# Kernel tuning notes

Hardware: AMD Instinct MI355X
Metric: run time of the kernel (lower is better)

## Reference

```python
import jax, jax.numpy as jnp
import numpy as np

DIM = 768
H = 12
HD = DIM // H
SCALE = HD ** (-0.5)


def setup_inputs() -> dict:
    key = jax.random.key(0)
    ks = jax.random.split(key, 10)
    s = DIM ** (-0.5)
    x = jax.random.normal(ks[0], (8, 1024, DIM), dtype=jnp.float32)
    Wq = jax.random.normal(ks[1], (DIM, DIM), dtype=jnp.float32) * s
    Wk = jax.random.normal(ks[2], (DIM, DIM), dtype=jnp.float32) * s
    Wv = jax.random.normal(ks[3], (DIM, DIM), dtype=jnp.float32) * s
    Wl = jax.random.normal(ks[4], (H, H), dtype=jnp.float32) * (H ** -0.5)
    bl = jax.random.normal(ks[5], (H,), dtype=jnp.float32) * 0.02
    Ww = jax.random.normal(ks[6], (H, H), dtype=jnp.float32) * (H ** -0.5)
    bw = jax.random.normal(ks[7], (H,), dtype=jnp.float32) * 0.02
    Wp = jax.random.normal(ks[8], (DIM, DIM), dtype=jnp.float32) * s
    bp = jax.random.normal(ks[9], (DIM,), dtype=jnp.float32) * 0.02
    return {"x": x, "Wq": Wq, "Wk": Wk, "Wv": Wv, "Wl": Wl, "bl": bl,
            "Ww": Ww, "bw": bw, "Wp": Wp, "bp": bp}


def reference(x, Wq, Wk, Wv, Wl, bl, Ww, bw, Wp, bp):
    B, N, C = x.shape
    # QKV projections (no bias), split heads -> (B, H, N, hd)
    q = (x @ Wq).reshape(B, N, H, HD).transpose(0, 2, 1, 3) * SCALE
    k = (x @ Wk).reshape(B, N, H, HD).transpose(0, 2, 1, 3)
    v = (x @ Wv).reshape(B, N, H, HD).transpose(0, 2, 1, 3)
    # scores: (B, H, N, N)
    attn = jnp.einsum('bhid,bhjd->bhij', q, k)
    # talking heads pre-softmax: mix over head axis (Linear on last dim of BNNH)
    attn = jnp.einsum('bhij,gh->bgij', attn, Wl) + bl[None, :, None, None]
    attn = jax.nn.softmax(attn, axis=-1)
    # talking heads post-softmax
    attn = jnp.einsum('bhij,gh->bgij', attn, Ww) + bw[None, :, None, None]
    out = jnp.einsum('bhij,bhjd->bhid', attn, v)  # (B, H, N, hd)
    out = out.transpose(0, 2, 1, 3).reshape(B, N, C)
    return out @ Wp + bp
```

## Files before the change

### kernel.cpp

```cpp
#include <hip/hip_runtime.h>
#include <hip/hip_bf16.h>

#define DIM 768
#define NH 12
#define HD 64
#define SEQ 1024
#define BATCH 8

typedef __bf16 bf16x8 __attribute__((ext_vector_type(8)));
typedef _Float16 f16x4 __attribute__((ext_vector_type(4)));
typedef float f32x4 __attribute__((ext_vector_type(4)));

__global__ __launch_bounds__(256) void xcvt(
    const float* __restrict__ X, __bf16* __restrict__ Xb)
{
  const size_t i = ((size_t)blockIdx.x * 256 + threadIdx.x) * 8;
  float4 a0 = *(const float4*)(X + i);
  float4 a1 = *(const float4*)(X + i + 4);
  bf16x8 v = { (__bf16)a0.x, (__bf16)a0.y, (__bf16)a0.z, (__bf16)a0.w,
               (__bf16)a1.x, (__bf16)a1.y, (__bf16)a1.z, (__bf16)a1.w };
  *(bf16x8*)(Xb + i) = v;
}

__global__ __launch_bounds__(256) void wtrans(
    const float* __restrict__ Wq, const float* __restrict__ Wk,
    const float* __restrict__ Wv, const float* __restrict__ Wp,
    __bf16* __restrict__ Tq, __bf16* __restrict__ Tk,
    __bf16* __restrict__ Tv, __bf16* __restrict__ Tp)
{
  const int z = blockIdx.z;
  const float* W = (z==0) ? Wq : (z==1) ? Wk : (z==2) ? Wv : Wp;
  __bf16* T = (z==0) ? Tq : (z==1) ? Tk : (z==2) ? Tv : Tp;
  __shared__ float tile[32][33];
  const int t = threadIdx.x, tx = t & 31, ty = t >> 5;
  const int k0 = blockIdx.y * 32, n0 = blockIdx.x * 32;
#pragma unroll
  for (int u = 0; u < 4; ++u)
    tile[ty + u*8][tx] = W[(size_t)(k0 + ty + u*8) * DIM + n0 + tx];
  __syncthreads();
#pragma unroll
  for (int u = 0; u < 4; ++u)
    T[(size_t)(n0 + ty + u*8) * DIM + k0 + tx] = (__bf16)tile[tx][ty + u*8];
}

__global__ __launch_bounds__(256) void gemm_qkv(
    const __bf16* __restrict__ Xb, const __bf16* __restrict__ WT,
    __bf16* __restrict__ Qo, __bf16* __restrict__ Ko, _Float16* __restrict__ Vt2)
{
  __shared__ __bf16 As[128 * 40];
  __shared__ __bf16 Bs[128 * 40];

  const int t = threadIdx.x, lane = t & 63, w = t >> 6;
  const int n16 = lane & 15, q = lane >> 4;
  const int m0 = blockIdx.y * 128, n0 = blockIdx.x * 128;
  const int wm = (w >> 1) * 64, wn = (w & 1) * 64;

  const int srow = t >> 2, scol = (t & 3) * 8;
  const __bf16* Ag = Xb + (size_t)(m0 + srow) * DIM + scol;
  const __bf16* Bg = WT + (size_t)(n0 + srow) * DIM + scol;

  f32x4 acc[4][4];
#pragma unroll
  for (int mt = 0; mt < 4; ++mt)
#pragma unroll
    for (int nt = 0; nt < 4; ++nt) acc[mt][nt] = (f32x4){0.f,0.f,0.f,0.f};

  for (int kb = 0; kb < DIM; kb += 32) {
    __syncthreads();
    bf16x8 a0 = *(const bf16x8*)(Ag + kb);
    bf16x8 a1 = *(const bf16x8*)(Ag + (size_t)64 * DIM + kb);
    bf16x8 b0 = *(const bf16x8*)(Bg + kb);
    bf16x8 b1 = *(const bf16x8*)(Bg + (size_t)64 * DIM + kb);
    *(bf16x8*)&As[srow * 40 + scol] = a0;
    *(bf16x8*)&As[(srow + 64) * 40 + scol] = a1;
    *(bf16x8*)&Bs[srow * 40 + scol] = b0;
    *(bf16x8*)&Bs[(srow + 64) * 40 + scol] = b1;
    __syncthreads();

    bf16x8 af[4], bg[4];
#pragma unroll
    for (int mt = 0; mt < 4; ++mt)
      af[mt] = *(const bf16x8*)&As[(wm + mt*16 + n16) * 40 + q*8];
#pragma unroll
    for (int nt = 0; nt < 4; ++nt)
      bg[nt] = *(const bf16x8*)&Bs[(wn + nt*16 + n16) * 40 + q*8];
#pragma unroll
    for (int mt = 0; mt < 4; ++mt)
#pragma unroll
      for (int nt = 0; nt < 4; ++nt)
        acc[mt][nt] = __builtin_amdgcn_mfma_f32_16x16x32_bf16(af[mt], bg[nt], acc[mt][nt], 0, 0, 0);
  }

#pragma unroll
  for (int nt = 0; nt < 4; ++nt) {
    const int n = n0 + wn + nt*16 + n16;
    const int z = n / DIM, c = n % DIM;
    const int h = c >> 6, d = c & 63;
#pragma unroll
    for (int mt = 0; mt < 4; ++mt) {
#pragma unroll
      for (int r = 0; r < 4; ++r) {
        const int row = m0 + wm + mt*16 + q*4 + r;
        const int bb = row >> 10, ii = row & 1023;
        const float v = acc[mt][nt][r];
        if (z == 0)
          Qo[(((size_t)bb*NH + h)*SEQ + ii)*HD + d] = (__bf16)(v * 0.125f);
        else if (z == 1)
          Ko[(((size_t)bb*NH + h)*SEQ + ii)*HD + d] = (__bf16)v;
        else
          Vt2[((((size_t)bb*NH + h)*64 + (ii >> 4))*HD + d)*16 + (ii & 15)] = (_Float16)v;
      }
    }
  }
}

__global__ __launch_bounds__(256, 2) void attn_fused(
    const __bf16* __restrict__ Qg, const __bf16* __restrict__ Kg,
    const _Float16* __restrict__ Vt2,
    const float* __restrict__ Wl, const float* __restrict__ bl,
    const float* __restrict__ Ww, const float* __restrict__ bw,
    __bf16* __restrict__ Aout)
{
  __shared__ float Sl[2][12][324];
  __shared__ _Float16 Pl[2][16 * 248];

  const int t = threadIdx.x, lane = t & 63, w = t >> 6;
  const int n16 = lane & 15, q = lane >> 4;
  const int h0 = w * 3;
  const int b = blockIdx.y, i0 = blockIdx.x * 16;
  const size_t bbase = (size_t)b * NH * SEQ * HD;

  f16x4 wlA, wwA;
  f32x4 blC, bwC;
#pragma unroll
  for (int j = 0; j < 4; ++j) {
    const int k = q*4 + j;
    wlA[j] = (n16 < 12 && k < 12) ? (_Float16)Wl[n16*12 + k] : (_Float16)0.f;
    wwA[j] = (n16 < 12 && k < 12) ? (_Float16)Ww[n16*12 + k] : (_Float16)0.f;
    blC[j] = (k < 12) ? bl[k] : 0.f;
    bwC[j] = (k < 12) ? bw[k] : 0.f;
  }

  bf16x8 qf[3][2];
#pragma unroll
  for (int hh = 0; hh < 3; ++hh)
#pragma unroll
    for (int cc = 0; cc < 2; ++cc)
      qf[hh][cc] = *(const bf16x8*)(Qg + bbase + ((size_t)(h0+hh)*SEQ + i0 + n16)*HD + cc*32 + q*8);

  const f32x4 z4 = {0.f, 0.f, 0.f, 0.f};

  float lrun[4][4];
#pragma unroll
  for (int c = 0; c < 4; ++c)
#pragma unroll
    for (int r = 0; r < 4; ++r) lrun[c][r] = 0.f;

  bf16x8 kC[3][2], kN[3][2];
#pragma unroll
  for (int hh = 0; hh < 3; ++hh) {
    const __bf16* kp = Kg + bbase + ((size_t)(h0+hh)*SEQ + n16)*HD + q*8;
    kC[hh][0] = *(const bf16x8*)kp;
    kC[hh][1] = *(const bf16x8*)(kp + 32);
  }

#pragma unroll 2
  for (int jt = 0; jt < SEQ/16; ++jt) {
    const int buf = jt & 1;
    const int jn = (jt < SEQ/16 - 1) ? jt + 1 : jt;
#pragma unroll
    for (int hh = 0; hh < 3; ++hh) {
      const __bf16* kp = Kg + bbase + ((size_t)(h0+hh)*SEQ + jn*16 + n16)*HD + q*8;
      kN[hh][0] = *(const bf16x8*)kp;
      kN[hh][1] = *(const bf16x8*)(kp + 32);
    }
#pragma unroll
    for (int hh = 0; hh < 3; ++hh) {
      f32x4 s = __builtin_amdgcn_mfma_f32_16x16x32_bf16(kC[hh][0], qf[hh][0], z4, 0, 0, 0);
      s = __builtin_amdgcn_mfma_f32_16x16x32_bf16(kC[hh][1], qf[hh][1], s, 0, 0, 0);
      *(f32x4*)&Sl[buf][h0+hh][n16*20 + q*4] = s;
    }
    __syncthreads();
#pragma unroll
    for (int c = 0; c < 4; ++c) {
      const int i = w*4 + c;
      f16x4 sf;
#pragma unroll
      for (int dd = 0; dd < 4; ++dd) {
        int h = q*4 + dd; if (h > 11) h = 11;
        sf[dd] = (_Float16)Sl[buf][h][i*20 + n16];
      }
      f32x4 sm = __builtin_amdgcn_mfma_f32_16x16x16f16(wlA, sf, blC, 0, 0, 0);
#pragma unroll
      for (int r = 0; r < 4; ++r) lrun[c][r] += __expf(sm[r]);
    }
#pragma unroll
    for (int hh = 0; hh < 3; ++hh) { kC[hh][0] = kN[hh][0]; kC[hh][1] = kN[hh][1]; }
  }

  float linv[4][4];
#pragma unroll
  for (int c = 0; c < 4; ++c)
#pragma unroll
    for (int r = 0; r < 4; ++r) {
      float l = lrun[c][r];
      l += __shfl_xor(l, 1);
      l += __shfl_xor(l, 2);
      l += __shfl_xor(l, 4);
      l += __shfl_xor(l, 8);
      linv[c][r] = 1.0f / l;
    }

  f32x4 oacc[3][4];
#pragma unroll
  for (int hh = 0; hh < 3; ++hh)
#pragma unroll
    for (int dc = 0; dc < 4; ++dc) oacc[hh][dc] = z4;

  f16x4 vC[3][4], vN[3][4];
#pragma unroll
  for (int hh = 0; hh < 3; ++hh) {
    const __bf16* kp = Kg + bbase + ((size_t)(h0+hh)*SEQ + n16)*HD + q*8;
    kC[hh][0] = *(const bf16x8*)kp;
    kC[hh][1] = *(const bf16x8*)(kp + 32);
  }

#pragma unroll 2
  for (int jt = 0; jt < SEQ/16; ++jt) {
    const int buf = jt & 1;
    const int jn = (jt < SEQ/16 - 1) ? jt + 1 : jt;
#pragma unroll
    for (int hh = 0; hh < 3; ++hh) {
      const __bf16* kp = Kg + bbase + ((size_t)(h0+hh)*SEQ + jn*16 + n16)*HD + q*8;
      kN[hh][0] = *(const bf16x8*)kp;
      kN[hh][1] = *(const bf16x8*)(kp + 32);
    }
#pragma unroll
    for (int hh = 0; hh < 3; ++hh) {
      const _Float16* vb = Vt2 + (((size_t)(b*NH + h0 + hh)*64 + jt)*HD)*16;
#pragma unroll
      for (int dc = 0; dc < 4; ++dc)
        vN[hh][dc] = *(const f16x4*)(vb + (size_t)(dc*16 + n16)*16 + q*4);
    }
#pragma unroll
    for (int hh = 0; hh < 3; ++hh) {
      f32x4 s = __builtin_amdgcn_mfma_f32_16x16x32_bf16(kC[hh][0], qf[hh][0], z4, 0, 0, 0);
      s = __builtin_amdgcn_mfma_f32_16x16x32_bf16(kC[hh][1], qf[hh][1], s, 0, 0, 0);
      *(f32x4*)&Sl[buf][h0+hh][n16*20 + q*4] = s;
    }
    __syncthreads();
#pragma unroll
    for (int c = 0; c < 4; ++c) {
      const int i = w*4 + c;
      f16x4 sf;
#pragma unroll
      for (int dd = 0; dd < 4; ++dd) {
        int h = q*4 + dd; if (h > 11) h = 11;
        sf[dd] = (_Float16)Sl[buf][h][i*20 + n16];
      }
      f32x4 sm = __builtin_amdgcn_mfma_f32_16x16x16f16(wlA, sf, blC, 0, 0, 0);
      f16x4 pnf;
#pragma unroll
      for (int r = 0; r < 4; ++r)
        pnf[r] = (_Float16)(__expf(sm[r]) * linv[c][r]);
      f32x4 p2 = __builtin_amdgcn_mfma_f32_16x16x16f16(wwA, pnf, bwC, 0, 0, 0);
      if (q < 3) {
#pragma unroll
        for (int r = 0; r < 4; ++r)
          Pl[buf][i*248 + (q*4 + r)*20 + n16] = (_Float16)p2[r];
      }
    }
    if (jt > 0) {
#pragma unroll
      for (int hh = 0; hh < 3; ++hh) {
        const int g2 = h0 + hh;
        f16x4 pa = *(const f16x4*)&Pl[1 - buf][n16*248 + g2*20 + q*4];
#pragma unroll
        for (int dc = 0; dc < 4; ++dc)
          oacc[hh][dc] = __builtin_amdgcn_mfma_f32_16x16x16f16(pa, vC[hh][dc], oacc[hh][dc], 0, 0, 0);
      }
    }
#pragma unroll
    for (int hh = 0; hh < 3; ++hh) {
      kC[hh][0] = kN[hh][0]; kC[hh][1] = kN[hh][1];
#pragma unroll
      for (int dc = 0; dc < 4; ++dc) vC[hh][dc] = vN[hh][dc];
    }
  }
  __syncthreads();
#pragma unroll
  for (int hh = 0; hh < 3; ++hh) {
    const int g2 = h0 + hh;
    f16x4 pa = *(const f16x4*)&Pl[1][n16*248 + g2*20 + q*4];
#pragma unroll
    for (int dc = 0; dc < 4; ++dc)
      oacc[hh][dc] = __builtin_amdgcn_mfma_f32_16x16x16f16(pa, vC[hh][dc], oacc[hh][dc], 0, 0, 0);
  }

#pragma unroll
  for (int hh = 0; hh < 3; ++hh)
#pragma unroll
    for (int dc = 0; dc < 4; ++dc)
#pragma unroll
      for (int r = 0; r < 4; ++r)
        Aout[((size_t)(b*SEQ + i0 + q*4 + r))*DIM + (h0+hh)*HD + dc*16 + n16] =
            (__bf16)oacc[hh][dc][r];
}

__global__ __launch_bounds__(256) void gemm_proj(
    const __bf16* __restrict__ A, const __bf16* __restrict__ WpT,
    const float* __restrict__ bp, float* __restrict__ Out)
{
  __shared__ __bf16 As[128 * 40];
  __shared__ __bf16 Bs[128 * 40];

  const int t = threadIdx.x, lane = t & 63, w = t >> 6;
  const int n16 = lane & 15, q = lane >> 4;
  const int m0 = blockIdx.y * 128, n0 = blockIdx.x * 128;
  const int wm = (w >> 1) * 64, wn = (w & 1) * 64;

  const int srow = t >> 2, scol = (t & 3) * 8;
  const __bf16* Ag = A + (size_t)(m0 + srow) * DIM + scol;
  const __bf16* Bg = WpT + (size_t)(n0 + srow) * DIM + scol;

  f32x4 acc[4][4];
#pragma unroll
  for (int nt = 0; nt < 4; ++nt) {
    const float bpv = bp[n0 + wn + nt*16 + n16];
#pragma unroll
    for (int mt = 0; mt < 4; ++mt)
#pragma unroll
      for (int r = 0; r < 4; ++r) acc[mt][nt][r] = bpv;
  }

  for (int kb = 0; kb < DIM; kb += 32) {
    __syncthreads();
    bf16x8 a0 = *(const bf16x8*)(Ag + kb);
    bf16x8 a1 = *(const bf16x8*)(Ag + (size_t)64 * DIM + kb);
    bf16x8 b0 = *(const bf16x8*)(Bg + kb);
    bf16x8 b1 = *(const bf16x8*)(Bg + (size_t)64 * DIM + kb);
    *(bf16x8*)&As[srow * 40 + scol] = a0;
    *(bf16x8*)&As[(srow + 64) * 40 + scol] = a1;
    *(bf16x8*)&Bs[srow * 40 + scol] = b0;
    *(bf16x8*)&Bs[(srow + 64) * 40 + scol] = b1;
    __syncthreads();

    bf16x8 af[4], bg[4];
#pragma unroll
    for (int mt = 0; mt < 4; ++mt)
      af[mt] = *(const bf16x8*)&As[(wm + mt*16 + n16) * 40 + q*8];
#pragma unroll
    for (int nt = 0; nt < 4; ++nt)
      bg[nt] = *(const bf16x8*)&Bs[(wn + nt*16 + n16) * 40 + q*8];
#pragma unroll
    for (int mt = 0; mt < 4; ++mt)
#pragma unroll
      for (int nt = 0; nt < 4; ++nt)
        acc[mt][nt] = __builtin_amdgcn_mfma_f32_16x16x32_bf16(af[mt], bg[nt], acc[mt][nt], 0, 0, 0);
  }

#pragma unroll
  for (int nt = 0; nt < 4; ++nt) {
    const int n = n0 + wn + nt*16 + n16;
#pragma unroll
    for (int mt = 0; mt < 4; ++mt)
#pragma unroll
      for (int r = 0; r < 4; ++r) {
        const int row = m0 + wm + mt*16 + q*4 + r;
        Out[(size_t)row * DIM + n] = acc[mt][nt][r];
      }
  }
}

extern "C" void kernel_launch(void* const* d_in, const int* in_sizes, int n_in,
                              void* d_out, int out_size, void* d_ws, size_t ws_size,
                              hipStream_t stream) {
  const float* x  = (const float*)d_in[0];
  const float* Wq = (const float*)d_in[1];
  const float* Wk = (const float*)d_in[2];
  const float* Wv = (const float*)d_in[3];
  const float* Wl = (const float*)d_in[4];
  const float* bl = (const float*)d_in[5];
  const float* Ww = (const float*)d_in[6];
  const float* bw = (const float*)d_in[7];
  const float* Wp = (const float*)d_in[8];
  const float* bp = (const float*)d_in[9];

  char* p = (char*)d_ws;
  const size_t WSZ = (size_t)DIM * DIM * 2;
  const size_t TSZ = (size_t)BATCH * NH * SEQ * HD * 2;
  __bf16*   WqT = (__bf16*)p;            p += WSZ;
  __bf16*   WkT = (__bf16*)p;            p += WSZ;
  __bf16*   WvT = (__bf16*)p;            p += WSZ;
  __bf16*   WpT = (__bf16*)p;            p += WSZ;
  __bf16*   Q   = (__bf16*)p;            p += TSZ;
  __bf16*   K   = (__bf16*)p;            p += TSZ;
  _Float16* V2  = (_Float16*)p;          p += TSZ;
  __bf16*   AO  = (__bf16*)p;            p += TSZ;
  __bf16*   Xb  = (__bf16*)p;            p += TSZ;

  xcvt<<<dim3((BATCH*SEQ*DIM)/(256*8)), 256, 0, stream>>>(x, Xb);
  wtrans<<<dim3(24, 24, 4), 256, 0, stream>>>(Wq, Wk, Wv, Wp, WqT, WkT, WvT, WpT);
  gemm_qkv<<<dim3(18, 64), 256, 0, stream>>>(Xb, WqT, Q, K, V2);
  attn_fused<<<dim3(SEQ/16, BATCH), 256, 0, stream>>>(Q, K, V2, Wl, bl, Ww, bw, AO);
  gemm_proj<<<dim3(6, 64), 256, 0, stream>>>(AO, WpT, bp, (float*)d_out);
}
```

Measured before the change: 434.2 us.

## Split fused attention into key-split sum and PV kernels for more parallelism

The single fused attention kernel, launched as 512 blocks, becomes two kernels. The first computes softmax denominators over four key chunks and writes partial sums. The second does the P·V pass over two key chunks and writes two fp16 partial outputs, which the projection GEMM adds while loading its tiles. This raises block count and occupancy on a GPU that was underfilled. It also stores scores in fp16 shared memory, uses exp2 with log2e folded into the weights, and switches the projection to fp16 MFMA. In exchange the QK^T scores are recomputed across more blocks and there is extra partial-buffer traffic. Ap1 reuses the Xb buffer, and fp16 partial outputs add precision risk.

```diff
diff --git a/kernel.cpp b/kernel.cpp
--- a/kernel.cpp
+++ b/kernel.cpp
@@ -6,9 +6,13 @@
 #define HD 64
 #define SEQ 1024
 #define BATCH 8
+#define JSPA 4
+#define JSPB 2
+#define LOG2E 1.44269504f
 
 typedef __bf16 bf16x8 __attribute__((ext_vector_type(8)));
 typedef _Float16 f16x4 __attribute__((ext_vector_type(4)));
+typedef _Float16 f16x8 __attribute__((ext_vector_type(8)));
 typedef float f32x4 __attribute__((ext_vector_type(4)));
 
 __global__ __launch_bounds__(256) void xcvt(
@@ -26,11 +30,10 @@
     const float* __restrict__ Wq, const float* __restrict__ Wk,
     const float* __restrict__ Wv, const float* __restrict__ Wp,
     __bf16* __restrict__ Tq, __bf16* __restrict__ Tk,
-    __bf16* __restrict__ Tv, __bf16* __restrict__ Tp)
+    __bf16* __restrict__ Tv, _Float16* __restrict__ Tp)
 {
   const int z = blockIdx.z;
   const float* W = (z==0) ? Wq : (z==1) ? Wk : (z==2) ? Wv : Wp;
-  __bf16* T = (z==0) ? Tq : (z==1) ? Tk : (z==2) ? Tv : Tp;
   __shared__ float tile[32][33];
   const int t = threadIdx.x, tx = t & 31, ty = t >> 5;
   const int k0 = blockIdx.y * 32, n0 = blockIdx.x * 32;
@@ -38,9 +41,16 @@
   for (int u = 0; u < 4; ++u)
     tile[ty + u*8][tx] = W[(size_t)(k0 + ty + u*8) * DIM + n0 + tx];
   __syncthreads();
-#pragma unroll
-  for (int u = 0; u < 4; ++u)
-    T[(size_t)(n0 + ty + u*8) * DIM + k0 + tx] = (__bf16)tile[tx][ty + u*8];
+  if (z == 3) {
+#pragma unroll
+    for (int u = 0; u < 4; ++u)
+      Tp[(size_t)(n0 + ty + u*8) * DIM + k0 + tx] = (_Float16)tile[tx][ty + u*8];
+  } else {
+    __bf16* T = (z==0) ? Tq : (z==1) ? Tk : Tv;
+#pragma unroll
+    for (int u = 0; u < 4; ++u)
+      T[(size_t)(n0 + ty + u*8) * DIM + k0 + tx] = (__bf16)tile[tx][ty + u*8];
+  }
 }
 
 __global__ __launch_bounds__(256) void gemm_qkv(
@@ -114,31 +124,27 @@
   }
 }
 
-__global__ __launch_bounds__(256, 2) void attn_fused(
+__global__ __launch_bounds__(256, 4) void attn_sums(
     const __bf16* __restrict__ Qg, const __bf16* __restrict__ Kg,
-    const _Float16* __restrict__ Vt2,
     const float* __restrict__ Wl, const float* __restrict__ bl,
-    const float* __restrict__ Ww, const float* __restrict__ bw,
-    __bf16* __restrict__ Aout)
-{
-  __shared__ float Sl[2][12][324];
-  __shared__ _Float16 Pl[2][16 * 248];
+    float* __restrict__ lpart)
+{
+  __shared__ _Float16 Sl[2][12][324];
 
   const int t = threadIdx.x, lane = t & 63, w = t >> 6;
   const int n16 = lane & 15, q = lane >> 4;
   const int h0 = w * 3;
-  const int b = blockIdx.y, i0 = blockIdx.x * 16;
+  const int b = blockIdx.y, i0 = blockIdx.x * 16, z = blockIdx.z;
+  const int jt0 = z * (SEQ/16/JSPA), jt1 = jt0 + SEQ/16/JSPA;
   const size_t bbase = (size_t)b * NH * SEQ * HD;
 
-  f16x4 wlA, wwA;
-  f32x4 blC, bwC;
+  f16x4 wlA;
+  f32x4 blC;
 #pragma unroll
   for (int j = 0; j < 4; ++j) {
     const int k = q*4 + j;
-    wlA[j] = (n16 < 12 && k < 12) ? (_Float16)Wl[n16*12 + k] : (_Float16)0.f;
-    wwA[j] = (n16 < 12 && k < 12) ? (_Float16)Ww[n16*12 + k] : (_Float16)0.f;
-    blC[j] = (k < 12) ? bl[k] : 0.f;
-    bwC[j] = (k < 12) ? bw[k] : 0.f;
+    wlA[j] = (n16 < 12 && k < 12) ? (_Float16)(Wl[n16*12 + k] * LOG2E) : (_Float16)0.f;
+    blC[j] = (k < 12) ? bl[k] * LOG2E : 0.f;
   }
 
   bf16x8 qf[3][2];
@@ -159,15 +165,15 @@
   bf16x8 kC[3][2], kN[3][2];
 #pragma unroll
   for (int hh = 0; hh < 3; ++hh) {
-    const __bf16* kp = Kg + bbase + ((size_t)(h0+hh)*SEQ + n16)*HD + q*8;
+    const __bf16* kp = Kg + bbase + ((size_t)(h0+hh)*SEQ + jt0*16 + n16)*HD + q*8;
     kC[hh][0] = *(const bf16x8*)kp;
     kC[hh][1] = *(const bf16x8*)(kp + 32);
   }
 
 #pragma unroll 2
-  for (int jt = 0; jt < SEQ/16; ++jt) {
+  for (int jt = jt0; jt < jt1; ++jt) {
     const int buf = jt & 1;
-    const int jn = (jt < SEQ/16 - 1) ? jt + 1 : jt;
+    const int jn = (jt < jt1 - 1) ? jt + 1 : jt;
 #pragma unroll
     for (int hh = 0; hh < 3; ++hh) {
       const __bf16* kp = Kg + bbase + ((size_t)(h0+hh)*SEQ + jn*16 + n16)*HD + q*8;
@@ -178,7 +184,8 @@
     for (int hh = 0; hh < 3; ++hh) {
       f32x4 s = __builtin_amdgcn_mfma_f32_16x16x32_bf16(kC[hh][0], qf[hh][0], z4, 0, 0, 0);
       s = __builtin_amdgcn_mfma_f32_16x16x32_bf16(kC[hh][1], qf[hh][1], s, 0, 0, 0);
-      *(f32x4*)&Sl[buf][h0+hh][n16*20 + q*4] = s;
+      f16x4 sh = { (_Float16)s[0], (_Float16)s[1], (_Float16)s[2], (_Float16)s[3] };
+      *(f16x4*)&Sl[buf][h0+hh][n16*20 + q*4] = sh;
     }
     __syncthreads();
 #pragma unroll
@@ -188,19 +195,19 @@
 #pragma unroll
       for (int dd = 0; dd < 4; ++dd) {
         int h = q*4 + dd; if (h > 11) h = 11;
-        sf[dd] = (_Float16)Sl[buf][h][i*20 + n16];
+        sf[dd] = Sl[buf][h][i*20 + n16];
       }
       f32x4 sm = __builtin_amdgcn_mfma_f32_16x16x16f16(wlA, sf, blC, 0, 0, 0);
 #pragma unroll
-      for (int r = 0; r < 4; ++r) lrun[c][r] += __expf(sm[r]);
+      for (int r = 0; r < 4; ++r) lrun[c][r] += __builtin_amdgcn_exp2f(sm[r]);
     }
 #pragma unroll
     for (int hh = 0; hh < 3; ++hh) { kC[hh][0] = kN[hh][0]; kC[hh][1] = kN[hh][1]; }
   }
 
-  float linv[4][4];
-#pragma unroll
-  for (int c = 0; c < 4; ++c)
+  const int tile = b * (SEQ/16) + blockIdx.x;
+#pragma unroll
+  for (int c = 0; c < 4; ++c) {
 #pragma unroll
     for (int r = 0; r < 4; ++r) {
       float l = lrun[c][r];
@@ -208,8 +215,68 @@
       l += __shfl_xor(l, 2);
       l += __shfl_xor(l, 4);
       l += __shfl_xor(l, 8);
-      linv[c][r] = 1.0f / l;
-    }
+      const int g = q*4 + r;
+      if (n16 == 0 && g < 12)
+        lpart[(((size_t)tile*JSPA + z)*12 + g)*16 + w*4 + c] = l;
+    }
+  }
+}
+
+__global__ __launch_bounds__(256, 3) void attn_pv(
+    const __bf16* __restrict__ Qg, const __bf16* __restrict__ Kg,
+    const _Float16* __restrict__ Vt2,
+    const float* __restrict__ Wl, const float* __restrict__ bl,
+    const float* __restrict__ Ww, const float* __restrict__ bw,
+    const float* __restrict__ lpart,
+    _Float16* __restrict__ Ap0, _Float16* __restrict__ Ap1)
+{
+  __shared__ _Float16 Sl[2][12][324];
+  __shared__ _Float16 Pl[2][16 * 248];
+
+  const int t = threadIdx.x, lane = t & 63, w = t >> 6;
+  const int n16 = lane & 15, q = lane >> 4;
+  const int h0 = w * 3;
+  const int b = blockIdx.y, i0 = blockIdx.x * 16, z = blockIdx.z;
+  const int jt0 = z * (SEQ/16/JSPB), jt1 = jt0 + SEQ/16/JSPB;
+  const size_t bbase = (size_t)b * NH * SEQ * HD;
+
+  f16x4 wlA, wwA;
+  f32x4 blC, bwC;
+#pragma unroll
+  for (int j = 0; j < 4; ++j) {
+    const int k = q*4 + j;
+    wlA[j] = (n16 < 12 && k < 12) ? (_Float16)(Wl[n16*12 + k] * LOG2E) : (_Float16)0.f;
+    wwA[j] = (n16 < 12 && k < 12) ? (_Float16)Ww[n16*12 + k] : (_Float16)0.f;
+    blC[j] = (k < 12) ? bl[k] * LOG2E : 0.f;
+    bwC[j] = (k < 12) ? bw[k] : 0.f;
+  }
+
+  const int tile = b * (SEQ/16) + blockIdx.x;
+  float linv[4][4];
+#pragma unroll
+  for (int c = 0; c < 4; ++c)
+#pragma unroll
+    for (int r = 0; r < 4; ++r) {
+      const int g = q*4 + r;
+      if (g < 12) {
+        float l = 0.f;
+#pragma unroll
+        for (int zz = 0; zz < JSPA; ++zz)
+          l += lpart[(((size_t)tile*JSPA + zz)*12 + g)*16 + w*4 + c];
+        linv[c][r] = 1.0f / l;
+      } else {
+        linv[c][r] = 0.f;
+      }
+    }
+
+  bf16x8 qf[3][2];
+#pragma unroll
+  for (int hh = 0; hh < 3; ++hh)
+#pragma unroll
+    for (int cc = 0; cc < 2; ++cc)
+      qf[hh][cc] = *(const bf16x8*)(Qg + bbase + ((size_t)(h0+hh)*SEQ + i0 + n16)*HD + cc*32 + q*8);
+
+  const f32x4 z4 = {0.f, 0.f, 0.f, 0.f};
 
   f32x4 oacc[3][4];
 #pragma unroll
@@ -217,18 +284,19 @@
 #pragma unroll
     for (int dc = 0; dc < 4; ++dc) oacc[hh][dc] = z4;
 
+  bf16x8 kC[3][2], kN[3][2];
   f16x4 vC[3][4], vN[3][4];
 #pragma unroll
   for (int hh = 0; hh < 3; ++hh) {
-    const __bf16* kp = Kg + bbase + ((size_t)(h0+hh)*SEQ + n16)*HD + q*8;
+    const __bf16* kp = Kg + bbase + ((size_t)(h0+hh)*SEQ + jt0*16 + n16)*HD + q*8;
     kC[hh][0] = *(const bf16x8*)kp;
     kC[hh][1] = *(const bf16x8*)(kp + 32);
   }
 
 #pragma unroll 2
-  for (int jt = 0; jt < SEQ/16; ++jt) {
+  for (int jt = jt0; jt < jt1; ++jt) {
     const int buf = jt & 1;
-    const int jn = (jt < SEQ/16 - 1) ? jt + 1 : jt;
+    const int jn = (jt < jt1 - 1) ? jt + 1 : jt;
 #pragma unroll
     for (int hh = 0; hh < 3; ++hh) {
       const __bf16* kp = Kg + bbase + ((size_t)(h0+hh)*SEQ + jn*16 + n16)*HD + q*8;
@@ -246,7 +314,8 @@
     for (int hh = 0; hh < 3; ++hh) {
       f32x4 s = __builtin_amdgcn_mfma_f32_16x16x32_bf16(kC[hh][0], qf[hh][0], z4, 0, 0, 0);
       s = __builtin_amdgcn_mfma_f32_16x16x32_bf16(kC[hh][1], qf[hh][1], s, 0, 0, 0);
-      *(f32x4*)&Sl[buf][h0+hh][n16*20 + q*4] = s;
+      f16x4 sh = { (_Float16)s[0], (_Float16)s[1], (_Float16)s[2], (_Float16)s[3] };
+      *(f16x4*)&Sl[buf][h0+hh][n16*20 + q*4] = sh;
     }
     __syncthreads();
 #pragma unroll
@@ -256,13 +325,13 @@
 #pragma unroll
       for (int dd = 0; dd < 4; ++dd) {
         int h = q*4 + dd; if (h > 11) h = 11;
-        sf[dd] = (_Float16)Sl[buf][h][i*20 + n16];
+        sf[dd] = Sl[buf][h][i*20 + n16];
       }
       f32x4 sm = __builtin_amdgcn_mfma_f32_16x16x16f16(wlA, sf, blC, 0, 0, 0);
       f16x4 pnf;
 #pragma unroll
       for (int r = 0; r < 4; ++r)
-        pnf[r] = (_Float16)(__expf(sm[r]) * linv[c][r]);
+        pnf[r] = (_Float16)(__builtin_amdgcn_exp2f(sm[r]) * linv[c][r]);
       f32x4 p2 = __builtin_amdgcn_mfma_f32_16x16x16f16(wwA, pnf, bwC, 0, 0, 0);
       if (q < 3) {
 #pragma unroll
@@ -270,7 +339,7 @@
           Pl[buf][i*248 + (q*4 + r)*20 + n16] = (_Float16)p2[r];
       }
     }
-    if (jt > 0) {
+    if (jt > jt0) {
 #pragma unroll
       for (int hh = 0; hh < 3; ++hh) {
         const int g2 = h0 + hh;
@@ -297,22 +366,24 @@
       oacc[hh][dc] = __builtin_amdgcn_mfma_f32_16x16x16f16(pa, vC[hh][dc], oacc[hh][dc], 0, 0, 0);
   }
 
+  _Float16* Ao = z ? Ap1 : Ap0;
 #pragma unroll
   for (int hh = 0; hh < 3; ++hh)
 #pragma unroll
     for (int dc = 0; dc < 4; ++dc)
 #pragma unroll
       for (int r = 0; r < 4; ++r)
-        Aout[((size_t)(b*SEQ + i0 + q*4 + r))*DIM + (h0+hh)*HD + dc*16 + n16] =
-            (__bf16)oacc[hh][dc][r];
+        Ao[((size_t)(b*SEQ + i0 + q*4 + r))*DIM + (h0+hh)*HD + dc*16 + n16] =
+            (_Float16)oacc[hh][dc][r];
 }
 
 __global__ __launch_bounds__(256) void gemm_proj(
-    const __bf16* __restrict__ A, const __bf16* __restrict__ WpT,
+    const _Float16* __restrict__ A0, const _Float16* __restrict__ A1,
+    const _Float16* __restrict__ WpT,
     const float* __restrict__ bp, float* __restrict__ Out)
 {
-  __shared__ __bf16 As[128 * 40];
-  __shared__ __bf16 Bs[128 * 40];
+  __shared__ _Float16 As[128 * 40];
+  __shared__ _Float16 Bs[128 * 40];
 
   const int t = threadIdx.x, lane = t & 63, w = t >> 6;
   const int n16 = lane & 15, q = lane >> 4;
@@ -320,8 +391,9 @@
   const int wm = (w >> 1) * 64, wn = (w & 1) * 64;
 
   const int srow = t >> 2, scol = (t & 3) * 8;
-  const __bf16* Ag = A + (size_t)(m0 + srow) * DIM + scol;
-  const __bf16* Bg = WpT + (size_t)(n0 + srow) * DIM + scol;
+  const _Float16* Ag0 = A0 + (size_t)(m0 + srow) * DIM + scol;
+  const _Float16* Ag1 = A1 + (size_t)(m0 + srow) * DIM + scol;
+  const _Float16* Bg = WpT + (size_t)(n0 + srow) * DIM + scol;
 
   f32x4 acc[4][4];
 #pragma unroll
@@ -335,28 +407,29 @@
 
   for (int kb = 0; kb < DIM; kb += 32) {
     __syncthreads();
-    bf16x8 a0 = *(const bf16x8*)(Ag + kb);
-    bf16x8 a1 = *(const bf16x8*)(Ag + (size_t)64 * DIM + kb);
-    bf16x8 b0 = *(const bf16x8*)(Bg + kb);
-    bf16x8 b1 = *(const bf16x8*)(Bg + (size_t)64 * DIM + kb);
-    *(bf16x8*)&As[srow * 40 + scol] = a0;
-    *(bf16x8*)&As[(srow + 64) * 40 + scol] = a1;
-    *(bf16x8*)&Bs[srow * 40 + scol] = b0;
-    *(bf16x8*)&Bs[(srow + 64) * 40 + scol] = b1;
-    __syncthreads();
-
-    bf16x8 af[4], bg[4];
-#pragma unroll
-    for (int mt = 0; mt < 4; ++mt)
-      af[mt] = *(const bf16x8*)&As[(wm + mt*16 + n16) * 40 + q*8];
+    f16x8 a0 = *(const f16x8*)(Ag0 + kb) + *(const f16x8*)(Ag1 + kb);
+    f16x8 a1 = *(const f16x8*)(Ag0 + (size_t)64 * DIM + kb) +
+               *(const f16x8*)(Ag1 + (size_t)64 * DIM + kb);
+    f16x8 b0 = *(const f16x8*)(Bg + kb);
+    f16x8 b1 = *(const f16x8*)(Bg + (size_t)64 * DIM + kb);
+    *(f16x8*)&As[srow * 40 + scol] = a0;
+    *(f16x8*)&As[(srow + 64) * 40 + scol] = a1;
+    *(f16x8*)&Bs[srow * 40 + scol] = b0;
+    *(f16x8*)&Bs[(srow + 64) * 40 + scol] = b1;
+    __syncthreads();
+
+    f16x8 af[4], bg[4];
+#pragma unroll
+    for (int mt = 0; mt < 4; ++mt)
+      af[mt] = *(const f16x8*)&As[(wm + mt*16 + n16) * 40 + q*8];
 #pragma unroll
     for (int nt = 0; nt < 4; ++nt)
-      bg[nt] = *(const bf16x8*)&Bs[(wn + nt*16 + n16) * 40 + q*8];
+      bg[nt] = *(const f16x8*)&Bs[(wn + nt*16 + n16) * 40 + q*8];
 #pragma unroll
     for (int mt = 0; mt < 4; ++mt)
 #pragma unroll
       for (int nt = 0; nt < 4; ++nt)
-        acc[mt][nt] = __builtin_amdgcn_mfma_f32_16x16x32_bf16(af[mt], bg[nt], acc[mt][nt], 0, 0, 0);
+        acc[mt][nt] = __builtin_amdgcn_mfma_f32_16x16x32_f16(af[mt], bg[nt], acc[mt][nt], 0, 0, 0);
   }
 
 #pragma unroll
@@ -389,19 +462,24 @@
   char* p = (char*)d_ws;
   const size_t WSZ = (size_t)DIM * DIM * 2;
   const size_t TSZ = (size_t)BATCH * NH * SEQ * HD * 2;
+  const size_t LSZ = (size_t)BATCH * (SEQ/16) * JSPA * 12 * 16 * 4;
   __bf16*   WqT = (__bf16*)p;            p += WSZ;
   __bf16*   WkT = (__bf16*)p;            p += WSZ;
   __bf16*   WvT = (__bf16*)p;            p += WSZ;
-  __bf16*   WpT = (__bf16*)p;            p += WSZ;
+  _Float16* WpT = (_Float16*)p;          p += WSZ;
   __bf16*   Q   = (__bf16*)p;            p += TSZ;
   __bf16*   K   = (__bf16*)p;            p += TSZ;
   _Float16* V2  = (_Float16*)p;          p += TSZ;
-  __bf16*   AO  = (__bf16*)p;            p += TSZ;
+  _Float16* Ap0 = (_Float16*)p;          p += TSZ;
   __bf16*   Xb  = (__bf16*)p;            p += TSZ;
+  float*    lpart = (float*)p;           p += LSZ;
+  _Float16* Ap1 = (_Float16*)Xb;
 
   xcvt<<<dim3((BATCH*SEQ*DIM)/(256*8)), 256, 0, stream>>>(x, Xb);
   wtrans<<<dim3(24, 24, 4), 256, 0, stream>>>(Wq, Wk, Wv, Wp, WqT, WkT, WvT, WpT);
   gemm_qkv<<<dim3(18, 64), 256, 0, stream>>>(Xb, WqT, Q, K, V2);
-  attn_fused<<<dim3(SEQ/16, BATCH), 256, 0, stream>>>(Q, K, V2, Wl, bl, Ww, bw, AO);
-  gemm_proj<<<dim3(6, 64), 256, 0, stream>>>(AO, WpT, bp, (float*)d_out);
-}
+  attn_sums<<<dim3(SEQ/16, BATCH, JSPA), 256, 0, stream>>>(Q, K, Wl, bl, lpart);
+  attn_pv<<<dim3(SEQ/16, BATCH, JSPB), 256, 0, stream>>>(Q, K, V2, Wl, bl, Ww, bw,
+                                                         lpart, Ap0, Ap1);
+  gemm_proj<<<dim3(6, 64), 256, 0, stream>>>(Ap0, Ap1, WpT, bp, (float*)d_out);
+}
```

Result: slower. 985.5 us (+127.0%).

## Restructure talking-heads attention into 32-key tiles with software-pipelined stages

Applied to the files above, without the earlier changes.

The attention kernel now processes 32 keys per iteration instead of 16 and software-pipelines the stages. Scores are computed for tile jt while the head-mix, exp and PV work for earlier tiles run, so only one barrier is needed per iteration. Scores are stored in LDS as fp16 in a head-contiguous layout, which allows vector f16x4 loads in place of scalar gathers and halves LDS footprint. Exp is done with exp2 and log2e folded into Wl/bl, and batch moves to grid x so blocks sharing K/V run together and get better L2 reuse. The trade-offs are more registers for the doubled K/V fragments and fp16 precision loss on the raw scores.

```diff
diff --git a/kernel.cpp b/kernel.cpp
--- a/kernel.cpp
+++ b/kernel.cpp
@@ -6,6 +6,13 @@
 #define HD 64
 #define SEQ 1024
 #define BATCH 8
+#define LOG2E 1.44269504f
+
+#define NT (SEQ/32)
+#define SROW 390
+#define SBUF (16*SROW)
+#define PROW 434
+#define PBUF (16*PROW)
 
 typedef __bf16 bf16x8 __attribute__((ext_vector_type(8)));
 typedef _Float16 f16x4 __attribute__((ext_vector_type(4)));
@@ -121,23 +128,28 @@
     const float* __restrict__ Ww, const float* __restrict__ bw,
     __bf16* __restrict__ Aout)
 {
-  __shared__ float Sl[2][12][324];
-  __shared__ _Float16 Pl[2][16 * 248];
+  __shared__ _Float16 Sl[2][SBUF];
+  __shared__ _Float16 Pl[2][PBUF];
 
   const int t = threadIdx.x, lane = t & 63, w = t >> 6;
   const int n16 = lane & 15, q = lane >> 4;
   const int h0 = w * 3;
-  const int b = blockIdx.y, i0 = blockIdx.x * 16;
+  const int b = blockIdx.x, i0 = blockIdx.y * 16;
   const size_t bbase = (size_t)b * NH * SEQ * HD;
+
+  {
+    float4* sz = (float4*)&Sl[0][0];
+    for (int k = t; k < (2*SBUF)/8; k += 256) sz[k] = (float4){0.f,0.f,0.f,0.f};
+  }
 
   f16x4 wlA, wwA;
   f32x4 blC, bwC;
 #pragma unroll
   for (int j = 0; j < 4; ++j) {
     const int k = q*4 + j;
-    wlA[j] = (n16 < 12 && k < 12) ? (_Float16)Wl[n16*12 + k] : (_Float16)0.f;
+    wlA[j] = (n16 < 12 && k < 12) ? (_Float16)(Wl[n16*12 + k] * LOG2E) : (_Float16)0.f;
     wwA[j] = (n16 < 12 && k < 12) ? (_Float16)Ww[n16*12 + k] : (_Float16)0.f;
-    blC[j] = (k < 12) ? bl[k] : 0.f;
+    blC[j] = (k < 12) ? bl[k] * LOG2E : 0.f;
     bwC[j] = (k < 12) ? bw[k] : 0.f;
   }
 
@@ -149,6 +161,9 @@
       qf[hh][cc] = *(const bf16x8*)(Qg + bbase + ((size_t)(h0+hh)*SEQ + i0 + n16)*HD + cc*32 + q*8);
 
   const f32x4 z4 = {0.f, 0.f, 0.f, 0.f};
+  bf16x8 kC[3][2][2];
+
+  __syncthreads();
 
   float lrun[4][4];
 #pragma unroll
@@ -156,46 +171,55 @@
 #pragma unroll
     for (int r = 0; r < 4; ++r) lrun[c][r] = 0.f;
 
-  bf16x8 kC[3][2], kN[3][2];
-#pragma unroll
-  for (int hh = 0; hh < 3; ++hh) {
-    const __bf16* kp = Kg + bbase + ((size_t)(h0+hh)*SEQ + n16)*HD + q*8;
-    kC[hh][0] = *(const bf16x8*)kp;
-    kC[hh][1] = *(const bf16x8*)(kp + 32);
-  }
-
 #pragma unroll 2
-  for (int jt = 0; jt < SEQ/16; ++jt) {
+  for (int jt = 0; jt < NT; ++jt) {
     const int buf = jt & 1;
-    const int jn = (jt < SEQ/16 - 1) ? jt + 1 : jt;
-#pragma unroll
-    for (int hh = 0; hh < 3; ++hh) {
-      const __bf16* kp = Kg + bbase + ((size_t)(h0+hh)*SEQ + jn*16 + n16)*HD + q*8;
-      kN[hh][0] = *(const bf16x8*)kp;
-      kN[hh][1] = *(const bf16x8*)(kp + 32);
-    }
-#pragma unroll
-    for (int hh = 0; hh < 3; ++hh) {
-      f32x4 s = __builtin_amdgcn_mfma_f32_16x16x32_bf16(kC[hh][0], qf[hh][0], z4, 0, 0, 0);
-      s = __builtin_amdgcn_mfma_f32_16x16x32_bf16(kC[hh][1], qf[hh][1], s, 0, 0, 0);
-      *(f32x4*)&Sl[buf][h0+hh][n16*20 + q*4] = s;
-    }
-    __syncthreads();
+#pragma unroll
+    for (int hh = 0; hh < 3; ++hh)
+#pragma unroll
+      for (int s = 0; s < 2; ++s) {
+        const __bf16* kp = Kg + bbase + ((size_t)(h0+hh)*SEQ + jt*32 + s*16 + n16)*HD + q*8;
+        kC[hh][s][0] = *(const bf16x8*)kp;
+        kC[hh][s][1] = *(const bf16x8*)(kp + 32);
+      }
+    if (jt >= 1) {
+      const int sb = 1 - buf;
+#pragma unroll
+      for (int c = 0; c < 4; ++c) {
+        const int i = w*4 + c;
+#pragma unroll
+        for (int s = 0; s < 2; ++s) {
+          f16x4 sf = *(const f16x4*)&Sl[sb][i*SROW + (n16 + 16*s)*12 + q*4];
+          f32x4 sm = __builtin_amdgcn_mfma_f32_16x16x16f16(wlA, sf, blC, 0, 0, 0);
+#pragma unroll
+          for (int r = 0; r < 4; ++r) lrun[c][r] += __builtin_amdgcn_exp2f(sm[r]);
+        }
+      }
+    }
+#pragma unroll
+    for (int hh = 0; hh < 3; ++hh)
+#pragma unroll
+      for (int s = 0; s < 2; ++s) {
+        f32x4 sv = __builtin_amdgcn_mfma_f32_16x16x32_bf16(kC[hh][s][0], qf[hh][0], z4, 0, 0, 0);
+        sv = __builtin_amdgcn_mfma_f32_16x16x32_bf16(kC[hh][s][1], qf[hh][1], sv, 0, 0, 0);
+#pragma unroll
+        for (int r = 0; r < 4; ++r)
+          Sl[buf][n16*SROW + (16*s + q*4 + r)*12 + h0 + hh] = (_Float16)sv[r];
+      }
+    __syncthreads();
+  }
+  {
 #pragma unroll
     for (int c = 0; c < 4; ++c) {
       const int i = w*4 + c;
-      f16x4 sf;
-#pragma unroll
-      for (int dd = 0; dd < 4; ++dd) {
-        int h = q*4 + dd; if (h > 11) h = 11;
-        sf[dd] = (_Float16)Sl[buf][h][i*20 + n16];
-      }
-      f32x4 sm = __builtin_amdgcn_mfma_f32_16x16x16f16(wlA, sf, blC, 0, 0, 0);
-#pragma unroll
-      for (int r = 0; r < 4; ++r) lrun[c][r] += __expf(sm[r]);
-    }
-#pragma unroll
-    for (int hh = 0; hh < 3; ++hh) { kC[hh][0] = kN[hh][0]; kC[hh][1] = kN[hh][1]; }
+#pragma unroll
+      for (int s = 0; s < 2; ++s) {
+        f16x4 sf = *(const f16x4*)&Sl[1][i*SROW + (n16 + 16*s)*12 + q*4];
+        f32x4 sm = __builtin_amdgcn_mfma_f32_16x16x16f16(wlA, sf, blC, 0, 0, 0);
+#pragma unroll
+        for (int r = 0; r < 4; ++r) lrun[c][r] += __builtin_amdgcn_exp2f(sm[r]);
+      }
+    }
   }
 
   float linv[4][4];
@@ -208,7 +232,7 @@
       l += __shfl_xor(l, 2);
       l += __shfl_xor(l, 4);
       l += __shfl_xor(l, 8);
-      linv[c][r] = 1.0f / l;
+      linv[c][r] = (q*4 + r < 12) ? (1.0f / l) : 0.f;
     }
 
   f32x4 oacc[3][4];
@@ -217,84 +241,133 @@
 #pragma unroll
     for (int dc = 0; dc < 4; ++dc) oacc[hh][dc] = z4;
 
-  f16x4 vC[3][4], vN[3][4];
-#pragma unroll
-  for (int hh = 0; hh < 3; ++hh) {
-    const __bf16* kp = Kg + bbase + ((size_t)(h0+hh)*SEQ + n16)*HD + q*8;
-    kC[hh][0] = *(const bf16x8*)kp;
-    kC[hh][1] = *(const bf16x8*)(kp + 32);
-  }
+  f16x4 vC[3][2][4];
 
 #pragma unroll 2
-  for (int jt = 0; jt < SEQ/16; ++jt) {
+  for (int jt = 0; jt < NT; ++jt) {
     const int buf = jt & 1;
-    const int jn = (jt < SEQ/16 - 1) ? jt + 1 : jt;
-#pragma unroll
-    for (int hh = 0; hh < 3; ++hh) {
-      const __bf16* kp = Kg + bbase + ((size_t)(h0+hh)*SEQ + jn*16 + n16)*HD + q*8;
-      kN[hh][0] = *(const bf16x8*)kp;
-      kN[hh][1] = *(const bf16x8*)(kp + 32);
-    }
-#pragma unroll
-    for (int hh = 0; hh < 3; ++hh) {
-      const _Float16* vb = Vt2 + (((size_t)(b*NH + h0 + hh)*64 + jt)*HD)*16;
-#pragma unroll
-      for (int dc = 0; dc < 4; ++dc)
-        vN[hh][dc] = *(const f16x4*)(vb + (size_t)(dc*16 + n16)*16 + q*4);
-    }
-#pragma unroll
-    for (int hh = 0; hh < 3; ++hh) {
-      f32x4 s = __builtin_amdgcn_mfma_f32_16x16x32_bf16(kC[hh][0], qf[hh][0], z4, 0, 0, 0);
-      s = __builtin_amdgcn_mfma_f32_16x16x32_bf16(kC[hh][1], qf[hh][1], s, 0, 0, 0);
-      *(f32x4*)&Sl[buf][h0+hh][n16*20 + q*4] = s;
-    }
-    __syncthreads();
+#pragma unroll
+    for (int hh = 0; hh < 3; ++hh)
+#pragma unroll
+      for (int s = 0; s < 2; ++s) {
+        const __bf16* kp = Kg + bbase + ((size_t)(h0+hh)*SEQ + jt*32 + s*16 + n16)*HD + q*8;
+        kC[hh][s][0] = *(const bf16x8*)kp;
+        kC[hh][s][1] = *(const bf16x8*)(kp + 32);
+      }
+    if (jt >= 2) {
+#pragma unroll
+      for (int hh = 0; hh < 3; ++hh)
+#pragma unroll
+        for (int s = 0; s < 2; ++s) {
+          const _Float16* vb = Vt2 + (((size_t)(b*NH + h0 + hh)*64 + (jt-2)*2 + s)*HD)*16;
+#pragma unroll
+          for (int dc = 0; dc < 4; ++dc)
+            vC[hh][s][dc] = *(const f16x4*)(vb + (dc*16 + n16)*16 + q*4);
+        }
+    }
+    if (jt >= 1) {
+      const int sb = 1 - buf;
+#pragma unroll
+      for (int c = 0; c < 4; ++c) {
+        const int i = w*4 + c;
+#pragma unroll
+        for (int s = 0; s < 2; ++s) {
+          f16x4 sf = *(const f16x4*)&Sl[sb][i*SROW + (n16 + 16*s)*12 + q*4];
+          f32x4 sm = __builtin_amdgcn_mfma_f32_16x16x16f16(wlA, sf, blC, 0, 0, 0);
+          f16x4 pnf;
+#pragma unroll
+          for (int r = 0; r < 4; ++r)
+            pnf[r] = (_Float16)(__builtin_amdgcn_exp2f(sm[r]) * linv[c][r]);
+          f32x4 p2 = __builtin_amdgcn_mfma_f32_16x16x16f16(wwA, pnf, bwC, 0, 0, 0);
+          if (q < 3) {
+#pragma unroll
+            for (int r = 0; r < 4; ++r)
+              Pl[buf][i*PROW + (q*4 + r)*36 + n16 + 16*s] = (_Float16)p2[r];
+          }
+        }
+      }
+    }
+    if (jt >= 2) {
+#pragma unroll
+      for (int hh = 0; hh < 3; ++hh)
+#pragma unroll
+        for (int s = 0; s < 2; ++s) {
+          f16x4 pa = *(const f16x4*)&Pl[1-buf][n16*PROW + (h0+hh)*36 + 16*s + q*4];
+#pragma unroll
+          for (int dc = 0; dc < 4; ++dc)
+            oacc[hh][dc] = __builtin_amdgcn_mfma_f32_16x16x16f16(pa, vC[hh][s][dc], oacc[hh][dc], 0, 0, 0);
+        }
+    }
+#pragma unroll
+    for (int hh = 0; hh < 3; ++hh)
+#pragma unroll
+      for (int s = 0; s < 2; ++s) {
+        f32x4 sv = __builtin_amdgcn_mfma_f32_16x16x32_bf16(kC[hh][s][0], qf[hh][0], z4, 0, 0, 0);
+        sv = __builtin_amdgcn_mfma_f32_16x16x32_bf16(kC[hh][s][1], qf[hh][1], sv, 0, 0, 0);
+#pragma unroll
+        for (int r = 0; r < 4; ++r)
+          Sl[buf][n16*SROW + (16*s + q*4 + r)*12 + h0 + hh] = (_Float16)sv[r];
+      }
+    __syncthreads();
+  }
+
+  {
+#pragma unroll
+    for (int hh = 0; hh < 3; ++hh)
+#pragma unroll
+      for (int s = 0; s < 2; ++s) {
+        const _Float16* vb = Vt2 + (((size_t)(b*NH + h0 + hh)*64 + (NT-2)*2 + s)*HD)*16;
+#pragma unroll
+        for (int dc = 0; dc < 4; ++dc)
+          vC[hh][s][dc] = *(const f16x4*)(vb + (dc*16 + n16)*16 + q*4);
+      }
 #pragma unroll
     for (int c = 0; c < 4; ++c) {
       const int i = w*4 + c;
-      f16x4 sf;
-#pragma unroll
-      for (int dd = 0; dd < 4; ++dd) {
-        int h = q*4 + dd; if (h > 11) h = 11;
-        sf[dd] = (_Float16)Sl[buf][h][i*20 + n16];
-      }
-      f32x4 sm = __builtin_amdgcn_mfma_f32_16x16x16f16(wlA, sf, blC, 0, 0, 0);
-      f16x4 pnf;
-#pragma unroll
-      for (int r = 0; r < 4; ++r)
-        pnf[r] = (_Float16)(__expf(sm[r]) * linv[c][r]);
-      f32x4 p2 = __builtin_amdgcn_mfma_f32_16x16x16f16(wwA, pnf, bwC, 0, 0, 0);
-      if (q < 3) {
+#pragma unroll
+      for (int s = 0; s < 2; ++s) {
+        f16x4 sf = *(const f16x4*)&Sl[1][i*SROW + (n16 + 16*s)*12 + q*4];
+        f32x4 sm = __builtin_amdgcn_mfma_f32_16x16x16f16(wlA, sf, blC, 0, 0, 0);
+        f16x4 pnf;
 #pragma unroll
         for (int r = 0; r < 4; ++r)
-          Pl[buf][i*248 + (q*4 + r)*20 + n16] = (_Float16)p2[r];
-      }
-    }
-    if (jt > 0) {
-#pragma unroll
-      for (int hh = 0; hh < 3; ++hh) {
-        const int g2 = h0 + hh;
-        f16x4 pa = *(const f16x4*)&Pl[1 - buf][n16*248 + g2*20 + q*4];
+          pnf[r] = (_Float16)(__builtin_amdgcn_exp2f(sm[r]) * linv[c][r]);
+        f32x4 p2 = __builtin_amdgcn_mfma_f32_16x16x16f16(wwA, pnf, bwC, 0, 0, 0);
+        if (q < 3) {
+#pragma unroll
+          for (int r = 0; r < 4; ++r)
+            Pl[0][i*PROW + (q*4 + r)*36 + n16 + 16*s] = (_Float16)p2[r];
+        }
+      }
+    }
+#pragma unroll
+    for (int hh = 0; hh < 3; ++hh)
+#pragma unroll
+      for (int s = 0; s < 2; ++s) {
+        f16x4 pa = *(const f16x4*)&Pl[1][n16*PROW + (h0+hh)*36 + 16*s + q*4];
 #pragma unroll
         for (int dc = 0; dc < 4; ++dc)
-          oacc[hh][dc] = __builtin_amdgcn_mfma_f32_16x16x16f16(pa, vC[hh][dc], oacc[hh][dc], 0, 0, 0);
-      }
-    }
-#pragma unroll
-    for (int hh = 0; hh < 3; ++hh) {
-      kC[hh][0] = kN[hh][0]; kC[hh][1] = kN[hh][1];
-#pragma unroll
-      for (int dc = 0; dc < 4; ++dc) vC[hh][dc] = vN[hh][dc];
-    }
-  }
-  __syncthreads();
-#pragma unroll
-  for (int hh = 0; hh < 3; ++hh) {
-    const int g2 = h0 + hh;
-    f16x4 pa = *(const f16x4*)&Pl[1][n16*248 + g2*20 + q*4];
-#pragma unroll
-    for (int dc = 0; dc < 4; ++dc)
-      oacc[hh][dc] = __builtin_amdgcn_mfma_f32_16x16x16f16(pa, vC[hh][dc], oacc[hh][dc], 0, 0, 0);
+          oacc[hh][dc] = __builtin_amdgcn_mfma_f32_16x16x16f16(pa, vC[hh][s][dc], oacc[hh][dc], 0, 0, 0);
+      }
+#pragma unroll
+    for (int hh = 0; hh < 3; ++hh)
+#pragma unroll
+      for (int s = 0; s < 2; ++s) {
+        const _Float16* vb = Vt2 + (((size_t)(b*NH + h0 + hh)*64 + (NT-1)*2 + s)*HD)*16;
+#pragma unroll
+        for (int dc = 0; dc < 4; ++dc)
+          vC[hh][s][dc] = *(const f16x4*)(vb + (dc*16 + n16)*16 + q*4);
+      }
+    __syncthreads();
+#pragma unroll
+    for (int hh = 0; hh < 3; ++hh)
+#pragma unroll
+      for (int s = 0; s < 2; ++s) {
+        f16x4 pa = *(const f16x4*)&Pl[0][n16*PROW + (h0+hh)*36 + 16*s + q*4];
+#pragma unroll
+        for (int dc = 0; dc < 4; ++dc)
+          oacc[hh][dc] = __builtin_amdgcn_mfma_f32_16x16x16f16(pa, vC[hh][s][dc], oacc[hh][dc], 0, 0, 0);
+      }
   }
 
 #pragma unroll
@@ -402,6 +475,6 @@
   xcvt<<<dim3((BATCH*SEQ*DIM)/(256*8)), 256, 0, stream>>>(x, Xb);
   wtrans<<<dim3(24, 24, 4), 256, 0, stream>>>(Wq, Wk, Wv, Wp, WqT, WkT, WvT, WpT);
   gemm_qkv<<<dim3(18, 64), 256, 0, stream>>>(Xb, WqT, Q, K, V2);
-  attn_fused<<<dim3(SEQ/16, BATCH), 256, 0, stream>>>(Q, K, V2, Wl, bl, Ww, bw, AO);
+  attn_fused<<<dim3(BATCH, SEQ/16), 256, 0, stream>>>(Q, K, V2, Wl, bl, Ww, bw, AO);
   gemm_proj<<<dim3(6, 64), 256, 0, stream>>>(AO, WpT, bp, (float*)d_out);
 }
```

Result: slower. 453.3 us (+4.4%).
